# Performance work log

Hardware: AMD Instinct MI355X
Metric: run time of the kernel (lower is better)

The kernel has to match this reference:

```python
import jax, jax.numpy as jnp
import numpy as np

B, S, D, H = 4, 2048, 1024, 16
DK = D // H


def setup_inputs() -> dict:
    key = jax.random.key(0)
    ks = jax.random.split(key, 10)
    std = 0.02
    inp = {
        "input": jax.random.normal(ks[0], (B, S, D), dtype=jnp.float32),
        "attention_reweight": jax.random.uniform(ks[1], (B, S), dtype=jnp.float32),
        "mask": 1,
        "Wq": jax.random.normal(ks[2], (D, D), dtype=jnp.float32) * std,
        "bq": jnp.zeros((D,), dtype=jnp.float32),
        "Wk": jax.random.normal(ks[3], (D, D), dtype=jnp.float32) * std,
        "bk": jnp.zeros((D,), dtype=jnp.float32),
        "Wv": jax.random.normal(ks[4], (D, D), dtype=jnp.float32) * std,
        "bv": jnp.zeros((D,), dtype=jnp.float32),
        "Wo": jax.random.normal(ks[5], (D, D), dtype=jnp.float32) * std,
        "bo": jnp.zeros((D,), dtype=jnp.float32),
    }
    return inp


def reference(input, attention_reweight, mask, Wq, bq, Wk, bk, Wv, bv, Wo, bo):
    b, s, d = input.shape
    # QKV projections (torch Linear: x @ W.T + b)
    q = (input @ Wq.T + bq).reshape(b, s, H, DK).transpose(0, 2, 1, 3)  # [B,H,S,dk]
    k = (input @ Wk.T + bk).reshape(b, s, H, DK).transpose(0, 2, 1, 3)
    v = (input @ Wv.T + bv).reshape(b, s, H, DK).transpose(0, 2, 1, 3)

    scores = jnp.einsum("bhqd,bhkd->bhqk", q, k)  # [B,H,S,S]
    if mask:
        causal = jnp.triu(jnp.ones((s, s), dtype=scores.dtype), k=1)
        scores = scores - causal * 1e9
    scores = scores / jnp.sqrt(jnp.asarray(DK, dtype=jnp.float32))
    # reweight per key position: [B,S] broadcast over heads and query positions
    scores = scores * attention_reweight[:, None, None, :]

    attn = jax.nn.softmax(scores, axis=-1)
    out = jnp.einsum("bhqk,bhkd->bhqd", attn, v)  # [B,H,S,dk]
    out = out.transpose(0, 2, 1, 3).reshape(b, s, d)
    return out @ Wo.T + bo
```

## Files before the change

kernel.cpp:

```cpp
#include <hip/hip_runtime.h>
#include <math.h>

#define B_  4
#define S_  2048
#define D_  1024
#define H_  16
#define DK_ 64

typedef __bf16 bf16x8 __attribute__((ext_vector_type(8)));
typedef float  f32x4  __attribute__((ext_vector_type(4)));

__device__ __forceinline__ unsigned short f2bf(float f) {
  unsigned int u = __builtin_bit_cast(unsigned int, f);
  u += 0x7fffu + ((u >> 16) & 1u);
  return (unsigned short)(u >> 16);
}

__device__ __forceinline__ unsigned short bfbits(float f) {
  __bf16 h = (__bf16)f;
  return __builtin_bit_cast(unsigned short, h);
}

__device__ __forceinline__ f32x4 mfma16(bf16x8 a, bf16x8 b, f32x4 c) {
  return __builtin_amdgcn_mfma_f32_16x16x32_bf16(a, b, c, 0, 0, 0);
}

__device__ __forceinline__ void gl_lds16(const unsigned short* g, unsigned short* l) {
  __builtin_amdgcn_global_load_lds(
      (const __attribute__((address_space(1))) void*)g,
      (__attribute__((address_space(3))) void*)l, 16, 0, 0);
}

__global__ void SAA_cast_bf16(const float* __restrict__ src,
                              unsigned short* __restrict__ dst, int n4) {
  int i = blockIdx.x * blockDim.x + threadIdx.x;
  int stride = gridDim.x * blockDim.x;
  for (; i < n4; i += stride) {
    float4 v = reinterpret_cast<const float4*>(src)[i];
    ushort4 o;
    o.x = f2bf(v.x); o.y = f2bf(v.y); o.z = f2bf(v.z); o.w = f2bf(v.w);
    reinterpret_cast<ushort4*>(dst)[i] = o;
  }
}

__global__ void SAA_cast4(const float* __restrict__ s0, const float* __restrict__ s1,
                          const float* __restrict__ s2, const float* __restrict__ s3,
                          unsigned short* __restrict__ d0, unsigned short* __restrict__ d1,
                          unsigned short* __restrict__ d2, unsigned short* __restrict__ d3)
{
  const int y = blockIdx.y;
  const float* src = (y == 0) ? s0 : (y == 1) ? s1 : (y == 2) ? s2 : s3;
  unsigned short* dst = (y == 0) ? d0 : (y == 1) ? d1 : (y == 2) ? d2 : d3;
  const int n4 = (D_ * D_) / 4;
  int i = blockIdx.x * blockDim.x + threadIdx.x;
  int stride = gridDim.x * blockDim.x;
  for (; i < n4; i += stride) {
    float4 v = reinterpret_cast<const float4*>(src)[i];
    ushort4 o;
    o.x = f2bf(v.x); o.y = f2bf(v.y); o.z = f2bf(v.z); o.w = f2bf(v.w);
    reinterpret_cast<ushort4*>(dst)[i] = o;
  }
}

__global__ __launch_bounds__(512)
void SAA_gemm_qkv(const unsigned short* __restrict__ Xb,
                  const unsigned short* __restrict__ Wqb,
                  const unsigned short* __restrict__ Wkb,
                  const unsigned short* __restrict__ Wvb,
                  const float* __restrict__ bq,
                  const float* __restrict__ bk,
                  const float* __restrict__ bv,
                  const float* __restrict__ rw,
                  unsigned short* __restrict__ Qo,
                  unsigned short* __restrict__ Ko,
                  unsigned short* __restrict__ Vto)
{
  const int K = D_;
  __shared__ __attribute__((aligned(16))) unsigned short smem[40960];
#define sAp(sl)     (smem + (sl) * 8192)
#define sBp(sl, m)  (smem + 16384 + ((sl) * 3 + (m)) * 4096)

  const int t = threadIdx.x;
  const int w = t >> 6, l = t & 63;
  const int wm = w >> 2, wn = w & 3;
  const int lr = l & 15, lg = l >> 4;

  const int bid = blockIdx.x;
  const int m0 = (bid >> 3) * 256;
  const int n0 = (bid & 7) * 128;

  const unsigned short* gA  = Xb  + (size_t)m0 * K;
  const unsigned short* gB0 = Wqb + (size_t)n0 * K;
  const unsigned short* gB1 = Wkb + (size_t)n0 * K;
  const unsigned short* gB2 = Wvb + (size_t)n0 * K;

  int sarow[2], saoff[2];
#pragma unroll
  for (int i = 0; i < 2; i++) {
    const int c = i * 512 + t;
    sarow[i] = c >> 2;
    saoff[i] = ((c & 3) ^ ((sarow[i] >> 1) & 3)) * 8;
  }
  const int sbrow = t >> 2;
  const int sboff = ((t & 3) ^ ((sbrow >> 1) & 3)) * 8;

#define STAGE(s, k0)                                                          \
  do {                                                                        \
    _Pragma("unroll")                                                         \
    for (int i = 0; i < 2; i++)                                               \
      gl_lds16(gA + (size_t)sarow[i] * K + (k0) + saoff[i],                   \
               sAp(s) + (i * 512 + t) * 8);                                   \
    const size_t gob = (size_t)sbrow * K + (k0) + sboff;                      \
    gl_lds16(gB0 + gob, sBp(s, 0) + t * 8);                                   \
    gl_lds16(gB1 + gob, sBp(s, 1) + t * 8);                                   \
    gl_lds16(gB2 + gob, sBp(s, 2) + t * 8);                                   \
  } while (0)

  STAGE(0, 0);

  f32x4 acc[3][8][2] = {};

#pragma unroll 2
  for (int T = 0; T < 32; ++T) {
    __syncthreads();
    if (T + 1 < 32) STAGE((T + 1) & 1, (T + 1) * 32);

    const unsigned short* At = sAp(T & 1);
    bf16x8 afr[8];
#pragma unroll
    for (int mi = 0; mi < 8; ++mi) {
      const int row = wm * 128 + mi * 16 + lr;
      afr[mi] = *reinterpret_cast<const bf16x8*>(
          &At[row * 32 + ((lg ^ ((row >> 1) & 3)) << 3)]);
    }
#pragma unroll
    for (int mat = 0; mat < 3; ++mat) {
      const unsigned short* Bt = sBp(T & 1, mat);
      bf16x8 bfr[2];
#pragma unroll
      for (int n = 0; n < 2; ++n) {
        const int row = wn * 32 + n * 16 + lr;
        bfr[n] = *reinterpret_cast<const bf16x8*>(
            &Bt[row * 32 + ((lg ^ ((row >> 1) & 3)) << 3)]);
      }
#pragma unroll
      for (int mi = 0; mi < 8; ++mi)
#pragma unroll
        for (int n = 0; n < 2; ++n)
          acc[mat][mi][n] = mfma16(afr[mi], bfr[n], acc[mat][mi][n]);
    }
  }
#undef STAGE

  __syncthreads();

#pragma unroll
  for (int n = 0; n < 2; ++n) {
    const int col = n0 + wn * 32 + n * 16 + lr;
    const int h = col >> 6, dk = col & 63;
    const float bvv = bv[col];
#pragma unroll
    for (int mi = 0; mi < 8; ++mi) {
      const int row0 = m0 + wm * 128 + mi * 16 + lg * 4;
      const int b = row0 >> 11, s0 = row0 & 2047;
      ushort4 pk;
      pk.x = bfbits(acc[2][mi][n][0] + bvv);
      pk.y = bfbits(acc[2][mi][n][1] + bvv);
      pk.z = bfbits(acc[2][mi][n][2] + bvv);
      pk.w = bfbits(acc[2][mi][n][3] + bvv);
      *reinterpret_cast<ushort4*>(
          &Vto[(((size_t)b * H_ + h) * DK_ + dk) * S_ + s0]) = pk;
    }
  }

  unsigned short* bounce = smem;
  for (int mat = 0; mat < 2; ++mat) {
    const float* bias = mat ? bk : bq;
#pragma unroll
    for (int n = 0; n < 2; ++n) {
      const int col = n0 + wn * 32 + n * 16 + lr;
      const int lcol = wn * 32 + n * 16 + lr;
      const float bs = bias[col];
#pragma unroll
      for (int mi = 0; mi < 8; ++mi) {
#pragma unroll
        for (int r = 0; r < 4; ++r) {
          const int lrow = wm * 128 + mi * 16 + lg * 4 + r;
          float v = acc[mat][mi][n][r] + bs;
          if (mat) v *= 0.18033688011112042f * rw[m0 + lrow];
          bounce[lrow * 132 + lcol] = bfbits(v);
        }
      }
    }
    __syncthreads();
#pragma unroll
    for (int i = 0; i < 4; ++i) {
      const int idx = i * 512 + t;
      const int lrow = idx >> 3, c16 = (idx & 7) * 16;
      const int row = m0 + lrow;
      const int b = row >> 11, s = row & 2047;
      const int col = n0 + c16;
      const int h = col >> 6, dk = col & 63;
      const unsigned short* srcp = &bounce[lrow * 132 + c16];
      unsigned short* dst = (mat ? Ko : Qo) + (((size_t)b * H_ + h) * S_ + s) * DK_ + dk;
#pragma unroll
      for (int j = 0; j < 4; ++j)
        reinterpret_cast<ushort4*>(dst)[j] =
            reinterpret_cast<const ushort4*>(srcp)[j];
    }
    __syncthreads();
  }
#undef sAp
#undef sBp
}

__global__ __launch_bounds__(512)
void SAA_attn(const unsigned short* __restrict__ Q,
              const unsigned short* __restrict__ Kb,
              const unsigned short* __restrict__ Vt,
              const int* __restrict__ maskp,
              unsigned short* __restrict__ Cb)
{
  const int L = (blockIdx.x & 7) * 64 + (blockIdx.x >> 3);
  const int pairid = L & 7;
  const int h = (L >> 3) & 15;
  const int b = L >> 7;

  const int t = threadIdx.x, w = t >> 6, l = t & 63;
  const int lr = l & 15, lg = l >> 4;
  const int mask = maskp[0];

  __shared__ __attribute__((aligned(16))) unsigned short Kt[2][64 * 64];
  __shared__ __attribute__((aligned(16))) unsigned short Vl[2][64 * 64];
  __shared__ __attribute__((aligned(16))) unsigned short Pl[8][16 * 80];

  const size_t bh = (size_t)b * H_ + h;
  const unsigned short* Qbh = Q + bh * S_ * DK_;
  const unsigned short* Kbh = Kb + bh * S_ * DK_;
  const unsigned short* Vbh = Vt + bh * DK_ * S_;
  unsigned short* Pw = &Pl[w][0];

  const int r0 = t >> 3, cc0 = t & 7;
  const int sw0 = (cc0 ^ (r0 & 7)) * 8;

  for (int half = 0; half < 2; ++half) {
    const int qb = half ? (15 - pairid) : pairid;
    const int q0 = qb * 128;
    const int wq = q0 + w * 16;

    bf16x8 qf[2];
#pragma unroll
    for (int ks = 0; ks < 2; ks++)
      qf[ks] = *reinterpret_cast<const bf16x8*>(
          &Qbh[(size_t)(wq + lr) * DK_ + ks * 32 + lg * 8]);

    f32x4 acc[4] = {};
    float lrun[4] = {0.f, 0.f, 0.f, 0.f};

    const int nkt = mask ? (qb * 2 + 2) : (S_ / 64);
    const int wqmax = wq + 15;

    __syncthreads();

    gl_lds16(Kbh + (size_t)r0 * DK_ + sw0, &Kt[0][t * 8]);
    gl_lds16(Vbh + (size_t)r0 * S_ + sw0,  &Vl[0][t * 8]);
    int cur = 0;

    for (int kt = 0; kt < nkt; ++kt) {
      __syncthreads();
      if (kt + 1 < nkt) {
        const int kn = (kt + 1) * 64;
        const int nb = cur ^ 1;
        gl_lds16(Kbh + (size_t)(kn + r0) * DK_ + sw0, &Kt[nb][t * 8]);
        gl_lds16(Vbh + (size_t)r0 * S_ + kn + sw0,    &Vl[nb][t * 8]);
      }

      const int k0 = kt * 64;
      const bool active = (!mask) || (k0 <= wqmax);
      if (active) {
        const unsigned short* Kc = &Kt[cur][0];
        const unsigned short* Vc = &Vl[cur][0];

        __builtin_amdgcn_s_setprio(1);
        f32x4 sc[4] = {};
#pragma unroll
        for (int ks = 0; ks < 2; ++ks) {
          const int swk = (((ks * 4 + lg) ^ (lr & 7)) << 3);
#pragma unroll
          for (int t2 = 0; t2 < 4; ++t2) {
            bf16x8 kf = *reinterpret_cast<const bf16x8*>(&Kc[(t2 * 16 + lr) * 64 + swk]);
            sc[t2] = mfma16(qf[ks], kf, sc[t2]);
          }
        }
        __builtin_amdgcn_s_setprio(0);

        const bool needmask = mask && (k0 + 63 > wq);

#pragma unroll
        for (int r = 0; r < 4; r++) {
          const int row = wq + lg * 4 + r;
          float v0 = sc[0][r], v1 = sc[1][r];
          float v2 = sc[2][r], v3 = sc[3][r];
          if (needmask) {
            if (k0 + lr      > row) v0 = -1e30f;
            if (k0 + 16 + lr > row) v1 = -1e30f;
            if (k0 + 32 + lr > row) v2 = -1e30f;
            if (k0 + 48 + lr > row) v3 = -1e30f;
          }
          const float p0 = __builtin_amdgcn_exp2f(v0);
          const float p1 = __builtin_amdgcn_exp2f(v1);
          const float p2 = __builtin_amdgcn_exp2f(v2);
          const float p3 = __builtin_amdgcn_exp2f(v3);
          lrun[r] += (p0 + p1) + (p2 + p3);
          unsigned short* pp = &Pw[(lg * 4 + r) * 80 + lr];
          pp[0]  = bfbits(p0);
          pp[16] = bfbits(p1);
          pp[32] = bfbits(p2);
          pp[48] = bfbits(p3);
        }

        __builtin_amdgcn_s_setprio(1);
#pragma unroll
        for (int ks = 0; ks < 2; ++ks) {
          const int swk = (((ks * 4 + lg) ^ (lr & 7)) << 3);
          bf16x8 pf = *reinterpret_cast<const bf16x8*>(&Pw[lr * 80 + ks * 32 + lg * 8]);
#pragma unroll
          for (int dt = 0; dt < 4; ++dt) {
            bf16x8 vf = *reinterpret_cast<const bf16x8*>(&Vc[(dt * 16 + lr) * 64 + swk]);
            acc[dt] = mfma16(pf, vf, acc[dt]);
          }
        }
        __builtin_amdgcn_s_setprio(0);
      }
      cur ^= 1;
    }

#pragma unroll
    for (int r = 0; r < 4; r++) {
      float rs = lrun[r];
      rs += __shfl_xor(rs, 1);
      rs += __shfl_xor(rs, 2);
      rs += __shfl_xor(rs, 4);
      rs += __shfl_xor(rs, 8);
      lrun[r] = __builtin_amdgcn_rcpf(rs);
    }
#pragma unroll
    for (int dt = 0; dt < 4; dt++) {
#pragma unroll
      for (int r = 0; r < 4; r++) {
        const int row = wq + lg * 4 + r;
        const int col = h * DK_ + dt * 16 + lr;
        Cb[((size_t)b * S_ + row) * D_ + col] = bfbits(acc[dt][r] * lrun[r]);
      }
    }
  }
}

__global__ __launch_bounds__(512)
void SAA_gemm_out(const unsigned short* __restrict__ Cb,
                  const unsigned short* __restrict__ Wob,
                  const float* __restrict__ bo,
                  float* __restrict__ Y)
{
  const int K = D_;
  __shared__ __attribute__((aligned(16))) unsigned short lA[2][512 * 64];
  __shared__ __attribute__((aligned(16))) unsigned short lB[2][64 * 64];

  const int L = (blockIdx.x & 7) * 32 + (blockIdx.x >> 3);
  const int nx = L & 15, my = L >> 4;

  const int t = threadIdx.x;
  const int w = t >> 6, l = t & 63;
  const int lr = l & 15, lg = l >> 4;
  const int r7 = lr & 7;

  const int m0 = my * 512;
  const int n0 = nx * 64;

  const unsigned short* gA = Cb + (size_t)m0 * K;
  const unsigned short* gB = Wob + (size_t)n0 * K;

  const int sr = t >> 3;
  const int soff = ((t & 7) ^ (sr & 7)) * 8;

#define STAGEO(s, k0)                                                         \
  do {                                                                        \
    _Pragma("unroll")                                                         \
    for (int i = 0; i < 8; i++)                                               \
      gl_lds16(gA + (size_t)(i * 64 + sr) * K + (k0) + soff,                  \
               &lA[s][(i * 512 + t) * 8]);                                    \
    gl_lds16(gB + (size_t)sr * K + (k0) + soff, &lB[s][t * 8]);               \
  } while (0)

  STAGEO(0, 0);

  f32x4 acc[4][4] = {};

#pragma unroll 2
  for (int T = 0; T < 16; ++T) {
    __syncthreads();
    if (T + 1 < 16) STAGEO((T + 1) & 1, (T + 1) * 64);

    const unsigned short* At = lA[T & 1];
    const unsigned short* Bt = lB[T & 1];
#pragma unroll
    for (int ks = 0; ks < 2; ks++) {
      const int swk = (((ks * 4 + lg) ^ r7) << 3);
      bf16x8 af[4], bfr[4];
#pragma unroll
      for (int i = 0; i < 4; i++)
        af[i] = *reinterpret_cast<const bf16x8*>(&At[(w * 64 + i * 16 + lr) * 64 + swk]);
#pragma unroll
      for (int j = 0; j < 4; j++)
        bfr[j] = *reinterpret_cast<const bf16x8*>(&Bt[(j * 16 + lr) * 64 + swk]);
#pragma unroll
      for (int i = 0; i < 4; i++)
#pragma unroll
        for (int j = 0; j < 4; j++)
          acc[i][j] = mfma16(af[i], bfr[j], acc[i][j]);
    }
  }
#undef STAGEO

#pragma unroll
  for (int j = 0; j < 4; j++) {
    const int col = n0 + j * 16 + lr;
    const float bsv = bo[col];
#pragma unroll
    for (int i = 0; i < 4; i++) {
#pragma unroll
      for (int r = 0; r < 4; r++) {
        const int row = m0 + w * 64 + i * 16 + lg * 4 + r;
        Y[(size_t)row * D_ + col] = acc[i][j][r] + bsv;
      }
    }
  }
}

extern "C" void kernel_launch(void* const* d_in, const int* in_sizes, int n_in,
                              void* d_out, int out_size, void* d_ws, size_t ws_size,
                              hipStream_t stream) {
  const float* input = (const float*)d_in[0];
  const float* rw    = (const float*)d_in[1];
  const int*   maskp = (const int*)d_in[2];
  const float* Wq = (const float*)d_in[3];
  const float* bq = (const float*)d_in[4];
  const float* Wk = (const float*)d_in[5];
  const float* bk = (const float*)d_in[6];
  const float* Wv = (const float*)d_in[7];
  const float* bv = (const float*)d_in[8];
  const float* Wo = (const float*)d_in[9];
  const float* bo = (const float*)d_in[10];

  char* ws = (char*)d_ws;
  unsigned short* Xb  = (unsigned short*)(ws);
  unsigned short* Wqb = (unsigned short*)(ws + (16u << 20));
  unsigned short* Wkb = (unsigned short*)(ws + (18u << 20));
  unsigned short* Wvb = (unsigned short*)(ws + (20u << 20));
  unsigned short* Wob = (unsigned short*)(ws + (22u << 20));
  unsigned short* Qo  = (unsigned short*)(ws + (24u << 20));
  unsigned short* Ko  = (unsigned short*)(ws + (40u << 20));
  unsigned short* Vto = (unsigned short*)(ws + (56u << 20));
  unsigned short* Cb  = Xb;

  SAA_cast_bf16<<<2048, 256, 0, stream>>>(input, Xb, (B_ * S_ * D_) / 4);
  SAA_cast4<<<dim3(512, 4), 256, 0, stream>>>(Wq, Wk, Wv, Wo, Wqb, Wkb, Wvb, Wob);

  SAA_gemm_qkv<<<256, 512, 0, stream>>>(Xb, Wqb, Wkb, Wvb, bq, bk, bv, rw,
                                        Qo, Ko, Vto);
  SAA_attn<<<512, 512, 0, stream>>>(Qo, Ko, Vto, maskp, Cb);
  SAA_gemm_out<<<256, 512, 0, stream>>>(Cb, Wob, bo, (float*)d_out);
}
```

Baseline: 162.2 us.

## Merge cast kernels into one launch and XOR-swizzle attention P tile

The separate input cast and weight cast kernels are merged into one launch with a 5-row grid, where row 0 casts the activation tensor and rows 1-4 cast the weights. This removes one kernel launch. In the attention kernel, the per-wave P staging buffer drops from an 80-element padded row to an unpadded 64-element row with an XOR swizzle matching the V layout. This is meant to avoid LDS bank conflicts with less shared memory. A risk is that the input cast now runs on only 512 blocks instead of 2048, so that row does more serial work.

```diff
diff --git a/kernel.cpp b/kernel.cpp
--- a/kernel.cpp
+++ b/kernel.cpp
@@ -31,27 +31,17 @@
       (__attribute__((address_space(3))) void*)l, 16, 0, 0);
 }
 
-__global__ void SAA_cast_bf16(const float* __restrict__ src,
-                              unsigned short* __restrict__ dst, int n4) {
-  int i = blockIdx.x * blockDim.x + threadIdx.x;
-  int stride = gridDim.x * blockDim.x;
-  for (; i < n4; i += stride) {
-    float4 v = reinterpret_cast<const float4*>(src)[i];
-    ushort4 o;
-    o.x = f2bf(v.x); o.y = f2bf(v.y); o.z = f2bf(v.z); o.w = f2bf(v.w);
-    reinterpret_cast<ushort4*>(dst)[i] = o;
-  }
-}
-
-__global__ void SAA_cast4(const float* __restrict__ s0, const float* __restrict__ s1,
-                          const float* __restrict__ s2, const float* __restrict__ s3,
-                          unsigned short* __restrict__ d0, unsigned short* __restrict__ d1,
-                          unsigned short* __restrict__ d2, unsigned short* __restrict__ d3)
+__global__ void SAA_cast_all(const float* __restrict__ x,
+                             const float* __restrict__ s1, const float* __restrict__ s2,
+                             const float* __restrict__ s3, const float* __restrict__ s4,
+                             unsigned short* __restrict__ dx,
+                             unsigned short* __restrict__ d1, unsigned short* __restrict__ d2,
+                             unsigned short* __restrict__ d3, unsigned short* __restrict__ d4)
 {
   const int y = blockIdx.y;
-  const float* src = (y == 0) ? s0 : (y == 1) ? s1 : (y == 2) ? s2 : s3;
-  unsigned short* dst = (y == 0) ? d0 : (y == 1) ? d1 : (y == 2) ? d2 : d3;
-  const int n4 = (D_ * D_) / 4;
+  const float* src = (y == 0) ? x : (y == 1) ? s1 : (y == 2) ? s2 : (y == 3) ? s3 : s4;
+  unsigned short* dst = (y == 0) ? dx : (y == 1) ? d1 : (y == 2) ? d2 : (y == 3) ? d3 : d4;
+  const int n4 = (y == 0) ? (B_ * S_ * D_) / 4 : (D_ * D_) / 4;
   int i = blockIdx.x * blockDim.x + threadIdx.x;
   int stride = gridDim.x * blockDim.x;
   for (; i < n4; i += stride) {
@@ -232,7 +222,7 @@
 
   __shared__ __attribute__((aligned(16))) unsigned short Kt[2][64 * 64];
   __shared__ __attribute__((aligned(16))) unsigned short Vl[2][64 * 64];
-  __shared__ __attribute__((aligned(16))) unsigned short Pl[8][16 * 80];
+  __shared__ __attribute__((aligned(16))) unsigned short Pl[8][16 * 64];
 
   const size_t bh = (size_t)b * H_ + h;
   const unsigned short* Qbh = Q + bh * S_ * DK_;
@@ -312,18 +302,21 @@
           const float p2 = __builtin_amdgcn_exp2f(v2);
           const float p3 = __builtin_amdgcn_exp2f(v3);
           lrun[r] += (p0 + p1) + (p2 + p3);
-          unsigned short* pp = &Pw[(lg * 4 + r) * 80 + lr];
-          pp[0]  = bfbits(p0);
-          pp[16] = bfbits(p1);
-          pp[32] = bfbits(p2);
-          pp[48] = bfbits(p3);
+          const int prow = lg * 4 + r;
+          const int pr7 = prow & 7;
+          const int pbase = prow * 64 + (lr & 7);
+          const int hi = lr >> 3;
+          Pw[pbase + (((0 + hi) ^ pr7) << 3)] = bfbits(p0);
+          Pw[pbase + (((2 + hi) ^ pr7) << 3)] = bfbits(p1);
+          Pw[pbase + (((4 + hi) ^ pr7) << 3)] = bfbits(p2);
+          Pw[pbase + (((6 + hi) ^ pr7) << 3)] = bfbits(p3);
         }
 
         __builtin_amdgcn_s_setprio(1);
 #pragma unroll
         for (int ks = 0; ks < 2; ++ks) {
           const int swk = (((ks * 4 + lg) ^ (lr & 7)) << 3);
-          bf16x8 pf = *reinterpret_cast<const bf16x8*>(&Pw[lr * 80 + ks * 32 + lg * 8]);
+          bf16x8 pf = *reinterpret_cast<const bf16x8*>(&Pw[lr * 64 + swk]);
 #pragma unroll
           for (int dt = 0; dt < 4; ++dt) {
             bf16x8 vf = *reinterpret_cast<const bf16x8*>(&Vc[(dt * 16 + lr) * 64 + swk]);
@@ -463,8 +456,8 @@
   unsigned short* Vto = (unsigned short*)(ws + (56u << 20));
   unsigned short* Cb  = Xb;
 
-  SAA_cast_bf16<<<2048, 256, 0, stream>>>(input, Xb, (B_ * S_ * D_) / 4);
-  SAA_cast4<<<dim3(512, 4), 256, 0, stream>>>(Wq, Wk, Wv, Wo, Wqb, Wkb, Wvb, Wob);
+  SAA_cast_all<<<dim3(512, 5), 256, 0, stream>>>(input, Wq, Wk, Wv, Wo,
+                                                 Xb, Wqb, Wkb, Wvb, Wob);
 
   SAA_gemm_qkv<<<256, 512, 0, stream>>>(Xb, Wqb, Wkb, Wvb, bq, bk, bv, rw,
                                         Qo, Ko, Vto);
```

After: 160.7 us. No clear change (-0.9%).
